# Optimization experiments

Hardware: AMD Instinct MI355X
Metric: run time of the kernel (lower is better)

## Reference

```python
import jax, jax.numpy as jnp
import numpy as np

B = 2
ROW, COL = 63, 84          # resolution
ROW_, COL_ = 32, 42        # resolution_
N = ROW * COL              # 5292 kv tokens
N_ = ROW_ * COL_           # 1344 q tokens
IN_DIM, OUT_DIM = 256, 512
KEY_DIM, NUM_HEADS, ATTN_RATIO, STRIDE = 16, 8, 2, 2
D = ATTN_RATIO * KEY_DIM   # 32 (value dim per head)
DH = D * NUM_HEADS         # 256
NH_KD = KEY_DIM * NUM_HEADS  # 128
H_KV = DH + NH_KD          # 384
SCALE = KEY_DIM ** -0.5
EPS = 1e-5


def _build_bias_idxs():
    # replicates the itertools.product double loop, vectorized; ids ordered by
    # first occurrence in row-major scan (same as dict insertion order).
    r_ = np.arange(ROW_); c_ = np.arange(COL_)
    r = np.arange(ROW); c = np.arange(COL)
    off_r = np.abs(r_[:, None] * STRIDE - r[None, :])      # (32, 63)
    off_c = np.abs(c_[:, None] * STRIDE - c[None, :])      # (42, 84)
    keys = (off_r[:, None, :, None] * 1000 + off_c[None, :, None, :]).reshape(-1)
    _, first_idx, inv = np.unique(keys, return_index=True, return_inverse=True)
    order = np.argsort(first_idx)
    rank = np.empty_like(order); rank[order] = np.arange(len(order))
    idxs = rank[inv].reshape(N_, N).astype(np.int32)
    return idxs, len(order)


def setup_inputs() -> dict:
    key = jax.random.key(0)
    ks = jax.random.split(key, 12)
    idxs_np, n_off = _build_bias_idxs()
    inp = {
        "x": jax.random.normal(ks[0], (B, N, IN_DIM), jnp.float32),
        "kv_w": jax.random.normal(ks[1], (H_KV, IN_DIM), jnp.float32) * (IN_DIM ** -0.5),
        "kv_g": jnp.ones((H_KV,), jnp.float32),
        "kv_b": jnp.zeros((H_KV,), jnp.float32),
        "q_w": jax.random.normal(ks[2], (NH_KD, IN_DIM), jnp.float32) * (IN_DIM ** -0.5),
        "q_g": jnp.ones((NH_KD,), jnp.float32),
        "q_b": jnp.zeros((NH_KD,), jnp.float32),
        "proj_w": jax.random.normal(ks[3], (OUT_DIM, DH), jnp.float32) * (DH ** -0.5),
        "proj_g": jnp.ones((OUT_DIM,), jnp.float32),
        "proj_b": jnp.zeros((OUT_DIM,), jnp.float32),
        "bias_table": jax.random.normal(ks[4], (NUM_HEADS, n_off), jnp.float32) * 0.02,
        "bias_idxs": jnp.asarray(idxs_np),
    }
    return inp


def _linear_bn(x, w, g, b):
    # Linear (no bias) followed by BatchNorm1d in training mode (batch stats
    # over flattened (B*N) dim, biased variance).
    y = jnp.einsum("bnc,oc->bno", x, w)
    flat = y.reshape(-1, y.shape[-1])
    mu = flat.mean(0)
    var = flat.var(0)
    return (y - mu) * (g / jnp.sqrt(var + EPS)) + b


def _hardswish(x):
    return x * jnp.clip(x + 3.0, 0.0, 6.0) / 6.0


def reference(x, kv_w, kv_g, kv_b, q_w, q_g, q_b, proj_w, proj_g, proj_b,
              bias_table, bias_idxs):
    Bx = x.shape[0]
    # kv projection -> split k (KEY_DIM) and v (D) per head
    kv = _linear_bn(x, kv_w, kv_g, kv_b).reshape(Bx, N, NUM_HEADS, KEY_DIM + D)
    k = kv[..., :KEY_DIM].transpose(0, 2, 1, 3)   # (B, H, N, key_dim)
    v = kv[..., KEY_DIM:].transpose(0, 2, 1, 3)   # (B, H, N, d)
    # q: spatial subsample then projection
    xs = x.reshape(Bx, ROW, COL, IN_DIM)[:, ::STRIDE, ::STRIDE].reshape(Bx, N_, IN_DIM)
    q = _linear_bn(xs, q_w, q_g, q_b).reshape(Bx, N_, NUM_HEADS, KEY_DIM).transpose(0, 2, 1, 3)
    # gathered relative position bias: (H, N_, N)
    ab = bias_table[:, bias_idxs]
    attn = jnp.einsum("bhqd,bhkd->bhqk", q, k) * SCALE + ab[None]
    attn = jax.nn.softmax(attn, axis=-1)
    out = jnp.einsum("bhqk,bhkd->bhqd", attn, v)       # (B, H, N_, d)
    out = out.transpose(0, 2, 1, 3).reshape(Bx, N_, DH)
    out = _linear_bn(_hardswish(out), proj_w, proj_g, proj_b)
    return out
```

## Files before the change

### kernel.cpp

```cpp
#include <hip/hip_runtime.h>
#include <hip/hip_bf16.h>
#include <math.h>

#define N_K 5292
#define N_Q 1344
#define NH_KD 128
#define NROWS 21504
#define LOG2E 1.4426950408889634f
#define MSTAT 16.0f

typedef float f32x4 __attribute__((ext_vector_type(4)));
typedef short short8 __attribute__((ext_vector_type(8)));

__device__ __forceinline__ float fexp2(float x) {
#if __has_builtin(__builtin_amdgcn_exp2f)
    return __builtin_amdgcn_exp2f(x);
#else
    return exp2f(x);
#endif
}

__device__ __forceinline__ unsigned pk_bf16(float a, float b) {
    union { __hip_bfloat162 h; unsigned u; } c;
    c.h = __float22bfloat162_rn(make_float2(a, b));
    return c.u;
}
__device__ __forceinline__ unsigned short f2bf(float a) {
    return (unsigned short)pk_bf16(a, 0.f);
}

__global__ __launch_bounds__(256) void prep_kernel(
    const float* __restrict__ x, const float* __restrict__ kv_w,
    const float* __restrict__ q_w, const float* __restrict__ proj_w,
    const float* __restrict__ bias_table, const int* __restrict__ bias_idxs, int n_off,
    float* __restrict__ sums, unsigned short* __restrict__ Xp,
    unsigned short* __restrict__ Wp, float* __restrict__ bt_r)
{
    int bid = blockIdx.x;
    const int t = threadIdx.x;
    if (bid < 8) {
        int i = bid * 256 + t;
        if (i < 2048) sums[i] = 0.f;
        return;
    }
    bid -= 8;
    if (bid < 2646) {
        int i = bid * 256 + t;
        float4 v = ((const float4*)x)[i];
        ((uint2*)Xp)[i] = make_uint2(pk_bf16(v.x, v.y), pk_bf16(v.z, v.w));
        return;
    }
    bid -= 2646;
    if (bid < 256) {
        int i = bid * 256 + t;
        int j = i;
        const float* s;
        if (j < 384 * 64) s = kv_w;
        else if ((j -= 384 * 64) < 128 * 64) s = q_w;
        else { j -= 128 * 64; s = proj_w; }
        float4 v = ((const float4*)s)[j];
        ((uint2*)Wp)[i] = make_uint2(pk_bf16(v.x, v.y), pk_bf16(v.z, v.w));
        return;
    }
    bid -= 256;
    {
        int i = bid * 256 + t;
        if (i < 8 * N_K) {
            int h = i / N_K, j = i - h * N_K;
            bt_r[i] = fmaf(bias_table[h * n_off + bias_idxs[j]], LOG2E, -MSTAT);
        }
    }
}

__device__ __forceinline__ void gemm_body(
    const unsigned short* __restrict__ Ap, const unsigned short* __restrict__ Wp,
    long asrc, int nrow,
    unsigned short (*As)[40], unsigned short (*Bs)[40], f32x4 acc[4])
{
    const int t = threadIdx.x;
    const int w = t >> 6, lane = t & 63, g = lane >> 4, ln = lane & 15;
    const int srow = t >> 2;
    const int sc8 = (t & 3) * 8;

    for (int k0 = 0; k0 < 256; k0 += 32) {
        uint4 a = make_uint4(0, 0, 0, 0);
        if (asrc >= 0) a = *(const uint4*)(Ap + asrc * 256 + k0 + sc8);
        uint4 b = *(const uint4*)(Wp + (size_t)nrow * 256 + k0 + sc8);

        __syncthreads();
        *(uint4*)&As[srow][sc8] = a;
        *(uint4*)&Bs[srow][sc8] = b;
        __syncthreads();

        short8 ah = *(const short8*)&As[w * 16 + ln][g * 8];
        #pragma unroll
        for (int nt = 0; nt < 4; ++nt) {
            short8 bh = *(const short8*)&Bs[nt * 16 + ln][g * 8];
            acc[nt] = __builtin_amdgcn_mfma_f32_16x16x32_bf16(ah, bh, acc[nt], 0, 0, 0);
        }
    }
}

__device__ __forceinline__ void gemm_stats(f32x4 acc[4], float* __restrict__ sums,
                                           int n0, int Ncols, float* scratch)
{
    const int t = threadIdx.x;
    const int w = t >> 6, lane = t & 63, g = lane >> 4, ln = lane & 15;
    float s4[4], q4[4];
    #pragma unroll
    for (int nt = 0; nt < 4; ++nt) {
        float s = acc[nt][0] + acc[nt][1] + acc[nt][2] + acc[nt][3];
        float q = fmaf(acc[nt][0], acc[nt][0], fmaf(acc[nt][1], acc[nt][1],
                  fmaf(acc[nt][2], acc[nt][2], acc[nt][3] * acc[nt][3])));
        s += __shfl_xor(s, 16); s += __shfl_xor(s, 32);
        q += __shfl_xor(q, 16); q += __shfl_xor(q, 32);
        s4[nt] = s; q4[nt] = q;
    }
    __syncthreads();
    float* st_s = scratch;
    float* st_q = scratch + 256;
    if (g == 0) {
        #pragma unroll
        for (int nt = 0; nt < 4; ++nt) {
            st_s[(w * 4 + nt) * 16 + ln] = s4[nt];
            st_q[(w * 4 + nt) * 16 + ln] = q4[nt];
        }
    }
    __syncthreads();
    if (t < 64) {
        int nt = t >> 4, c = t & 15;
        float a = 0.f, b2 = 0.f;
        #pragma unroll
        for (int ww = 0; ww < 4; ++ww) {
            a  += st_s[(ww * 4 + nt) * 16 + c];
            b2 += st_q[(ww * 4 + nt) * 16 + c];
        }
        atomicAdd(&sums[n0 + nt * 16 + c], a);
        atomicAdd(&sums[Ncols + n0 + nt * 16 + c], b2);
    }
}

__global__ __launch_bounds__(256) void gemm_qkv(
    const unsigned short* __restrict__ Xp, const unsigned short* __restrict__ Wp,
    unsigned short* __restrict__ Kp, unsigned short* __restrict__ Vp,
    float* __restrict__ q_y, float* __restrict__ sums_kv, float* __restrict__ sums_q)
{
    __shared__ unsigned short As[64][40], Bs[64][40];
    const int t = threadIdx.x;
    const int w = t >> 6, lane = t & 63, g = lane >> 4, ln = lane & 15;
    const int srow = t >> 2;
    int id = blockIdx.x;

    f32x4 acc[4];
    #pragma unroll
    for (int nt = 0; nt < 4; ++nt) acc[nt] = (f32x4){0.f, 0.f, 0.f, 0.f};

    if (id < 1008) {
        const int xcd = id & 7, id8 = id >> 3;
        const int my = xcd + (id8 / 6) * 8, ny = id8 % 6;
        if (my >= 166) return;
        const int m0 = my * 64, n0 = ny * 64;
        int mrow = m0 + srow;
        long asrc = (mrow < 10584) ? mrow : -1;
        gemm_body(Xp, Wp, asrc, n0 + srow, As, Bs, acc);

        #pragma unroll
        for (int nt = 0; nt < 4; ++nt) {
            int c = n0 + nt * 16 + ln;
            int hh = c / 48, cc = c - 48 * hh;
            #pragma unroll
            for (int reg = 0; reg < 4; ++reg) {
                int mr = m0 + w * 16 + g * 4 + reg;
                if (mr < 10584) {
                    int bb = mr >= N_K;
                    int key = mr - bb * N_K;
                    unsigned short v16 = f2bf(acc[nt][reg]);
                    size_t slot = (size_t)(bb * 8 + hh) * N_K + key;
                    if (cc < 16) Kp[slot * 16 + cc] = v16;
                    else         Vp[slot * 32 + cc - 16] = v16;
                }
            }
        }
        gemm_stats(acc, sums_kv, n0, 384, (float*)&As[0][0]);
    } else {
        id -= 1008;
        const int xcd = id & 7, id8 = id >> 3;
        const int my = xcd + (id8 / 2) * 8, ny = id8 % 2;
        if (my >= 42) return;
        const int m0 = my * 64, n0 = ny * 64;
        int mrow = m0 + srow;
        long asrc = -1;
        {
            int bb = mrow / N_Q;
            int i = mrow - bb * N_Q;
            asrc = (long)(bb * N_K + (i / 42) * 168 + (i % 42) * 2);
        }
        gemm_body(Xp, Wp + 384 * 256, asrc, n0 + srow, As, Bs, acc);

        #pragma unroll
        for (int nt = 0; nt < 4; ++nt)
            #pragma unroll
            for (int reg = 0; reg < 4; ++reg) {
                int mr = m0 + w * 16 + g * 4 + reg;
                q_y[(size_t)mr * 128 + n0 + nt * 16 + ln] = acc[nt][reg];
            }
        gemm_stats(acc, sums_q, n0, 128, (float*)&As[0][0]);
    }
}

__global__ __launch_bounds__(256) void gemm_proj(
    const unsigned short* __restrict__ Ap, const unsigned short* __restrict__ Wp,
    float* __restrict__ Y, float* __restrict__ sums)
{
    __shared__ unsigned short As[64][40], Bs[64][40];
    const int t = threadIdx.x;
    const int w = t >> 6, lane = t & 63, g = lane >> 4, ln = lane & 15;
    const int id = blockIdx.x;
    const int xcd = id & 7, id8 = id >> 3;
    const int my = xcd + (id8 / 8) * 8, ny = id8 % 8;
    if (my >= 42) return;
    const int m0 = my * 64, n0 = ny * 64;

    f32x4 acc[4];
    #pragma unroll
    for (int nt = 0; nt < 4; ++nt) acc[nt] = (f32x4){0.f, 0.f, 0.f, 0.f};
    gemm_body(Ap, Wp, m0 + (t >> 2), n0 + (t >> 2), As, Bs, acc);

    #pragma unroll
    for (int nt = 0; nt < 4; ++nt)
        #pragma unroll
        for (int reg = 0; reg < 4; ++reg) {
            int mr = m0 + w * 16 + g * 4 + reg;
            Y[(size_t)mr * 512 + n0 + nt * 16 + ln] = acc[nt][reg];
        }
    gemm_stats(acc, sums, n0, 512, (float*)&As[0][0]);
}

__global__ __launch_bounds__(256, 5) void attn_mfma(
    const unsigned short* __restrict__ Kp, const unsigned short* __restrict__ Vp,
    const float* __restrict__ q_y, const float* __restrict__ sums_q,
    const float* __restrict__ q_g, const float* __restrict__ q_b,
    const float* __restrict__ sums_kv, const float* __restrict__ kv_g,
    const float* __restrict__ bt_r,
    float* __restrict__ pl, float* __restrict__ pacc)
{
    const int id = blockIdx.x;
    const int h = id & 7;
    const int z = (id >> 3) & 7;
    const int qt = id >> 6;
    const int b = z >> 2, ks = z & 3;
    const int t = threadIdx.x;
    const int w = t >> 6, lane = t & 63, g = lane >> 4, ln = lane & 15;

    __shared__ float bt_s[21 * 84];
    __shared__ unsigned short K_s[2][64][24];
    __shared__ unsigned short Vt_s[2][32][72];
    __shared__ unsigned short P_s[4][16][72];

    const int q0 = qt * 64;
    const int kstart = ks * 1344;
    const int kend = (kstart + 1344 < N_K) ? kstart + 1344 : N_K;
    const int ntiles = (kend - kstart + 63) >> 6;
    const bool tail = (ks == 3);

    const int kr0 = ks * 16;
    const int kr1 = (kend - 1) / 84;
    const int rq2min = (q0 / 42) * 2;
    const int rq2max = ((q0 + 63) / 42) * 2;
    int dr_lo = 0;
    if (rq2min > kr1) dr_lo = rq2min - kr1;
    else if (kr0 > rq2max) dr_lo = kr0 - rq2max;
    int a1 = rq2max - kr0, a2 = kr1 - rq2min;
    int dr_hi = a1 > a2 ? a1 : a2;
    {
        int nb = (dr_hi - dr_lo + 1) * 84;
        const float* src = bt_r + h * N_K + dr_lo * 84;
        for (int j = t; j < nb; j += 256) bt_s[j] = src[j];
    }

    short8 qfrag = (short8)0;
    if (lane < 32) {
        const float invq = 1.f / 2688.f, invk = 1.f / 10584.f;
        const float post = 0.25f * LOG2E;
        const int c0 = h * 16 + g * 8;
        const int ck = h * 48 + g * 8;
        const float* qp = q_y + (size_t)(b * N_Q + q0 + w * 16 + ln) * NH_KD + c0;
        float vv[8];
        #pragma unroll
        for (int j = 0; j < 8; ++j) {
            float mu  = sums_q[c0 + j] * invq;
            float var = fmaf(-mu, mu, sums_q[128 + c0 + j] * invq);
            float s   = q_g[c0 + j] * rsqrtf(var + 1e-5f) * post;
            float vq  = fmaf(qp[j], s, fmaf(-mu, s, q_b[c0 + j] * post));
            float muk = sums_kv[ck + j] * invk;
            float vrk = fmaf(-muk, muk, sums_kv[384 + ck + j] * invk);
            float sk  = kv_g[ck + j] * rsqrtf(vrk + 1e-5f);
            vv[j] = vq * sk;
        }
        union { short8 s; unsigned u[4]; } qf;
        qf.u[0] = pk_bf16(vv[0], vv[1]); qf.u[1] = pk_bf16(vv[2], vv[3]);
        qf.u[2] = pk_bf16(vv[4], vv[5]); qf.u[3] = pk_bf16(vv[6], vv[7]);
        qfrag = qf.s;
    }

    int rq2[4], cq2[4];
    #pragma unroll
    for (int reg = 0; reg < 4; ++reg) {
        int qg = q0 + w * 16 + g * 4 + reg;
        rq2[reg] = (qg / 42) * 2;
        cq2[reg] = (qg % 42) * 2;
    }
    int kr[4], kc[4];
    #pragma unroll
    for (int st = 0; st < 4; ++st) {
        int kg = kstart + st * 16 + ln;
        kr[st] = kg / 84;
        kc[st] = kg - kr[st] * 84;
    }

    const unsigned* kp_base = (const unsigned*)Kp + (size_t)(b * 8 + h) * N_K * 8;
    const unsigned* vp_base = (const unsigned*)Vp + (size_t)(b * 8 + h) * N_K * 16;
    const int skey = t >> 2, schunk = t & 3;
    const int vslot = ((skey & 15) << 2) | (skey >> 4);
    const int v0 = schunk * 8;

    uint2 kreg; uint4 vreg;
    {
        int kg = kstart + skey; if (kg > N_K - 1) kg = N_K - 1;
        kreg = *(const uint2*)(kp_base + (size_t)kg * 8 + schunk * 2);
        vreg = *(const uint4*)(vp_base + (size_t)kg * 16 + schunk * 4);
    }
    *(uint2*)&K_s[0][skey][schunk * 4] = kreg;
    Vt_s[0][v0 + 0][vslot] = (unsigned short)vreg.x;
    Vt_s[0][v0 + 1][vslot] = (unsigned short)(vreg.x >> 16);
    Vt_s[0][v0 + 2][vslot] = (unsigned short)vreg.y;
    Vt_s[0][v0 + 3][vslot] = (unsigned short)(vreg.y >> 16);
    Vt_s[0][v0 + 4][vslot] = (unsigned short)vreg.z;
    Vt_s[0][v0 + 5][vslot] = (unsigned short)(vreg.z >> 16);
    Vt_s[0][v0 + 6][vslot] = (unsigned short)vreg.w;
    Vt_s[0][v0 + 7][vslot] = (unsigned short)(vreg.w >> 16);
    __syncthreads();

    float l[4] = {0.f, 0.f, 0.f, 0.f};
    f32x4 acc0 = {0.f, 0.f, 0.f, 0.f}, acc1 = {0.f, 0.f, 0.f, 0.f};
    const f32x4 zero4 = {0.f, 0.f, 0.f, 0.f};
    int p = 0;

    for (int it = 0; it < ntiles; ++it) {
        const int k0 = kstart + it * 64;
        const bool notlast = (it + 1 < ntiles);
        if (notlast) {
            int kg = k0 + 64 + skey; if (kg > N_K - 1) kg = N_K - 1;
            kreg = *(const uint2*)(kp_base + (size_t)kg * 8 + schunk * 2);
            vreg = *(const uint4*)(vp_base + (size_t)kg * 16 + schunk * 4);
        }

        f32x4 sf[4];
        #pragma unroll
        for (int st = 0; st < 4; ++st) {
            short8 bf = (short8)0;
            if (lane < 32) bf = *(const short8*)&K_s[p][st * 16 + ln][g * 8];
            sf[st] = __builtin_amdgcn_mfma_f32_16x16x32_bf16(qfrag, bf, zero4, 0, 0, 0);
        }

        float pv[4][4];
        #pragma unroll
        for (int st = 0; st < 4; ++st) {
            #pragma unroll
            for (int reg = 0; reg < 4; ++reg) {
                int dr = rq2[reg] - kr[st]; dr = dr < 0 ? -dr : dr;
                int dc = cq2[reg] - kc[st]; dc = dc < 0 ? -dc : dc;
                pv[st][reg] = fexp2(sf[st][reg] + bt_s[(dr - dr_lo) * 84 + dc]);
            }
        }
        if (tail && it == ntiles - 1) {
            #pragma unroll
            for (int st = 0; st < 4; ++st) {
                bool bad = (k0 + st * 16 + ln) >= N_K;
                #pragma unroll
                for (int reg = 0; reg < 4; ++reg)
                    pv[st][reg] = bad ? 0.f : pv[st][reg];
            }
        }

        #pragma unroll
        for (int reg = 0; reg < 4; ++reg) {
            l[reg] += (pv[0][reg] + pv[1][reg]) + (pv[2][reg] + pv[3][reg]);
            uint2 pw = make_uint2(pk_bf16(pv[0][reg], pv[1][reg]),
                                  pk_bf16(pv[2][reg], pv[3][reg]));
            *(uint2*)&P_s[w][g * 4 + reg][4 * ln] = pw;
        }

        #pragma unroll
        for (int kt = 0; kt < 2; ++kt) {
            short8 af = *(const short8*)&P_s[w][ln][g * 8 + kt * 32];
            short8 b0 = *(const short8*)&Vt_s[p][ln][g * 8 + kt * 32];
            short8 b1 = *(const short8*)&Vt_s[p][ln + 16][g * 8 + kt * 32];
            acc0 = __builtin_amdgcn_mfma_f32_16x16x32_bf16(af, b0, acc0, 0, 0, 0);
            acc1 = __builtin_amdgcn_mfma_f32_16x16x32_bf16(af, b1, acc1, 0, 0, 0);
        }

        if (notlast) {
            int q2 = p ^ 1;
            *(uint2*)&K_s[q2][skey][schunk * 4] = kreg;
            Vt_s[q2][v0 + 0][vslot] = (unsigned short)vreg.x;
            Vt_s[q2][v0 + 1][vslot] = (unsigned short)(vreg.x >> 16);
            Vt_s[q2][v0 + 2][vslot] = (unsigned short)vreg.y;
            Vt_s[q2][v0 + 3][vslot] = (unsigned short)(vreg.y >> 16);
            Vt_s[q2][v0 + 4][vslot] = (unsigned short)vreg.z;
            Vt_s[q2][v0 + 5][vslot] = (unsigned short)(vreg.z >> 16);
            Vt_s[q2][v0 + 6][vslot] = (unsigned short)vreg.w;
            Vt_s[q2][v0 + 7][vslot] = (unsigned short)(vreg.w >> 16);
            __syncthreads();
            p = q2;
        }

        #pragma unroll
        for (int st = 0; st < 4; ++st) {
            kc[st] += 64;
            if (kc[st] >= 84) { kc[st] -= 84; kr[st] += 1; }
        }
    }

    #pragma unroll
    for (int reg = 0; reg < 4; ++reg) {
        float s = l[reg];
        s += __shfl_xor(s, 1, 16);
        s += __shfl_xor(s, 2, 16);
        s += __shfl_xor(s, 4, 16);
        s += __shfl_xor(s, 8, 16);
        l[reg] = s;
    }

    const int rbase = (b * 8 + h) * N_Q + q0 + w * 16;
    #pragma unroll
    for (int reg = 0; reg < 4; ++reg) {
        int prow = ks * NROWS + rbase + g * 4 + reg;
        pacc[(size_t)prow * 32 + ln]      = acc0[reg];
        pacc[(size_t)prow * 32 + 16 + ln] = acc1[reg];
        if (ln == 0) pl[prow] = l[reg];
    }
}

__global__ __launch_bounds__(256) void combine_kernel(const float* __restrict__ pl,
                                                      const float* __restrict__ pacc,
                                                      const float* __restrict__ sums_kv,
                                                      const float* __restrict__ kv_g,
                                                      const float* __restrict__ kv_b,
                                                      unsigned short* __restrict__ attn_o)
{
    int i = blockIdx.x * 256 + threadIdx.x;
    int r = i >> 5, e = i & 31;
    float L = (pl[r] + pl[NROWS + r]) + (pl[2 * NROWS + r] + pl[3 * NROWS + r]);
    float v = (pacc[(size_t)r * 32 + e] + pacc[(size_t)(NROWS + r) * 32 + e])
            + (pacc[(size_t)(2 * NROWS + r) * 32 + e] + pacc[(size_t)(3 * NROWS + r) * 32 + e]);
    int q = r % N_Q;
    int bh = r / N_Q;
    int hh = bh & 7, b = bh >> 3;
    const int ch = hh * 48 + 16 + e;
    const float invk = 1.f / 10584.f;
    float mu  = sums_kv[ch] * invk;
    float var = fmaf(-mu, mu, sums_kv[384 + ch] * invk);
    float s   = kv_g[ch] * rsqrtf(var + 1e-5f);
    float tt  = fmaf(-mu, s, kv_b[ch]);
    v = fmaf(s, v / L, tt);
    float hs = v * fminf(fmaxf(v + 3.f, 0.f), 6.f) * (1.f / 6.f);
    attn_o[(size_t)(b * N_Q + q) * 256 + hh * 32 + e] = f2bf(hs);
}

__global__ __launch_bounds__(256) void norm_apply(
    const float* __restrict__ Y, const float* __restrict__ sums,
    const float* __restrict__ g, const float* __restrict__ bb,
    float* __restrict__ out, int rows, int cols, float inv_rows)
{
    __shared__ float sc_s[64], sh_s[64];
    const int t = threadIdx.x;
    const int c0 = blockIdx.x * 64;
    if (t < 64) {
        int c = c0 + t;
        float mu  = sums[c] * inv_rows;
        float var = fmaf(-mu, mu, sums[cols + c] * inv_rows);
        float s   = g[c] * rsqrtf(var + 1e-5f);
        sc_s[t] = s;
        sh_s[t] = fmaf(-mu, s, bb[c]);
    }
    __syncthreads();
    const int c4 = (t & 15) * 4;
    float4 scv = *(const float4*)&sc_s[c4];
    float4 shv = *(const float4*)&sh_s[c4];
    for (int r = blockIdx.y * 16 + (t >> 4); r < rows; r += gridDim.y * 16) {
        size_t off = (size_t)r * cols + c0 + c4;
        float4 v = *(const float4*)(Y + off);
        v.x = fmaf(v.x, scv.x, shv.x);
        v.y = fmaf(v.y, scv.y, shv.y);
        v.z = fmaf(v.z, scv.z, shv.z);
        v.w = fmaf(v.w, scv.w, shv.w);
        *(float4*)(out + off) = v;
    }
}

extern "C" void kernel_launch(void* const* d_in, const int* in_sizes, int n_in,
                              void* d_out, int out_size, void* d_ws, size_t ws_size,
                              hipStream_t stream) {
    (void)n_in; (void)out_size; (void)ws_size;
    const float* x      = (const float*)d_in[0];
    const float* kv_w   = (const float*)d_in[1];
    const float* kv_g   = (const float*)d_in[2];
    const float* kv_b   = (const float*)d_in[3];
    const float* q_w    = (const float*)d_in[4];
    const float* q_g    = (const float*)d_in[5];
    const float* q_b    = (const float*)d_in[6];
    const float* proj_w = (const float*)d_in[7];
    const float* proj_g = (const float*)d_in[8];
    const float* proj_b = (const float*)d_in[9];
    const float* bias_table = (const float*)d_in[10];
    const int*   bias_idxs  = (const int*)d_in[11];
    const int    n_off = in_sizes[10] / 8;
    float* out = (float*)d_out;

    float* ws = (float*)d_ws;
    float* q_y  = ws;
    float* pacc = q_y + 2688 * 128;
    float* proj_y = pacc;
    float* pl = pacc + 4 * NROWS * 32;
    unsigned short* Xp = (unsigned short*)(pl + 4 * NROWS);
    unsigned short* Wp = Xp + 10584 * 256;
    unsigned short* attn_o = Wp + 1024 * 256;
    unsigned short* Kp = attn_o + 2688 * 256;
    unsigned short* Vp = Kp + 2 * 8 * N_K * 16;
    float* sums_kv = (float*)(Vp + 2 * 8 * N_K * 32);
    float* sums_q  = sums_kv + 768;
    float* sums_p  = sums_q + 256;
    float* bt_r    = sums_p + 1024;

    prep_kernel<<<3076, 256, 0, stream>>>(x, kv_w, q_w, proj_w, bias_table, bias_idxs,
                                          n_off, sums_kv, Xp, Wp, bt_r);
    gemm_qkv<<<1104, 256, 0, stream>>>(Xp, Wp, Kp, Vp, q_y, sums_kv, sums_q);
    attn_mfma<<<1344, 256, 0, stream>>>(Kp, Vp, q_y, sums_q, q_g, q_b,
                                        sums_kv, kv_g, bt_r, pl, pacc);
    combine_kernel<<<2688, 256, 0, stream>>>(pl, pacc, sums_kv, kv_g, kv_b, attn_o);
    gemm_proj<<<8 * 6 * 8, 256, 0, stream>>>(attn_o, Wp + 512 * 256, proj_y, sums_p);
    norm_apply<<<dim3(8, 84), 256, 0, stream>>>(proj_y, sums_p, proj_g, proj_b, out,
                                                2688, 512, 1.f / 2688.f);
}
```

Baseline: 210.6 us.

## Fuse bf16 casts into GEMMs, pre-transpose V, fold combine into attention

Removes the separate fp32-to-bf16 conversion of x and the weights from the prep kernel. The GEMMs now load fp32 and pack to bf16 in registers, which cuts one full read and write of x. The qkv GEMM epilogue writes V already transposed and permuted into a padded key layout, so the attention kernel can stage V with vector stores instead of scalar scatter into shared memory. The separate combine kernel is replaced by a last-block-done counter in the attention kernel, which then reduces the split-K partials and applies BN plus hardswish. This trades a launch and extra traffic for atomics, threadfences, and a scattered transposed V write.

New measurement: 341.6 us. 62.2% more time.

```diff
diff --git a/kernel.cpp b/kernel.cpp
--- a/kernel.cpp
+++ b/kernel.cpp
@@ -3,6 +3,7 @@
 #include <math.h>
 
 #define N_K 5292
+#define N_KP 5376
 #define N_Q 1344
 #define NH_KD 128
 #define NROWS 21504
@@ -30,39 +31,17 @@
 }
 
 __global__ __launch_bounds__(256) void prep_kernel(
-    const float* __restrict__ x, const float* __restrict__ kv_w,
-    const float* __restrict__ q_w, const float* __restrict__ proj_w,
     const float* __restrict__ bias_table, const int* __restrict__ bias_idxs, int n_off,
-    float* __restrict__ sums, unsigned short* __restrict__ Xp,
-    unsigned short* __restrict__ Wp, float* __restrict__ bt_r)
+    float* __restrict__ zbase, float* __restrict__ bt_r)
 {
     int bid = blockIdx.x;
     const int t = threadIdx.x;
-    if (bid < 8) {
+    if (bid < 10) {
         int i = bid * 256 + t;
-        if (i < 2048) sums[i] = 0.f;
+        if (i < 2560) zbase[i] = 0.f;
         return;
     }
-    bid -= 8;
-    if (bid < 2646) {
-        int i = bid * 256 + t;
-        float4 v = ((const float4*)x)[i];
-        ((uint2*)Xp)[i] = make_uint2(pk_bf16(v.x, v.y), pk_bf16(v.z, v.w));
-        return;
-    }
-    bid -= 2646;
-    if (bid < 256) {
-        int i = bid * 256 + t;
-        int j = i;
-        const float* s;
-        if (j < 384 * 64) s = kv_w;
-        else if ((j -= 384 * 64) < 128 * 64) s = q_w;
-        else { j -= 128 * 64; s = proj_w; }
-        float4 v = ((const float4*)s)[j];
-        ((uint2*)Wp)[i] = make_uint2(pk_bf16(v.x, v.y), pk_bf16(v.z, v.w));
-        return;
-    }
-    bid -= 256;
+    bid -= 10;
     {
         int i = bid * 256 + t;
         if (i < 8 * N_K) {
@@ -72,8 +51,8 @@
     }
 }
 
-__device__ __forceinline__ void gemm_body(
-    const unsigned short* __restrict__ Ap, const unsigned short* __restrict__ Wp,
+__device__ __forceinline__ void gemm_body_f32(
+    const float* __restrict__ A, const float* __restrict__ W,
     long asrc, int nrow,
     unsigned short (*As)[40], unsigned short (*Bs)[40], f32x4 acc[4])
 {
@@ -84,8 +63,47 @@
 
     for (int k0 = 0; k0 < 256; k0 += 32) {
         uint4 a = make_uint4(0, 0, 0, 0);
-        if (asrc >= 0) a = *(const uint4*)(Ap + asrc * 256 + k0 + sc8);
-        uint4 b = *(const uint4*)(Wp + (size_t)nrow * 256 + k0 + sc8);
+        if (asrc >= 0) {
+            float4 a0 = *(const float4*)(A + asrc * 256 + k0 + sc8);
+            float4 a1 = *(const float4*)(A + asrc * 256 + k0 + sc8 + 4);
+            a = make_uint4(pk_bf16(a0.x, a0.y), pk_bf16(a0.z, a0.w),
+                           pk_bf16(a1.x, a1.y), pk_bf16(a1.z, a1.w));
+        }
+        float4 b0 = *(const float4*)(W + (size_t)nrow * 256 + k0 + sc8);
+        float4 b1 = *(const float4*)(W + (size_t)nrow * 256 + k0 + sc8 + 4);
+        uint4 b = make_uint4(pk_bf16(b0.x, b0.y), pk_bf16(b0.z, b0.w),
+                             pk_bf16(b1.x, b1.y), pk_bf16(b1.z, b1.w));
+
+        __syncthreads();
+        *(uint4*)&As[srow][sc8] = a;
+        *(uint4*)&Bs[srow][sc8] = b;
+        __syncthreads();
+
+        short8 ah = *(const short8*)&As[w * 16 + ln][g * 8];
+        #pragma unroll
+        for (int nt = 0; nt < 4; ++nt) {
+            short8 bh = *(const short8*)&Bs[nt * 16 + ln][g * 8];
+            acc[nt] = __builtin_amdgcn_mfma_f32_16x16x32_bf16(ah, bh, acc[nt], 0, 0, 0);
+        }
+    }
+}
+
+__device__ __forceinline__ void gemm_body_bf16(
+    const unsigned short* __restrict__ A, const float* __restrict__ W,
+    long asrc, int nrow,
+    unsigned short (*As)[40], unsigned short (*Bs)[40], f32x4 acc[4])
+{
+    const int t = threadIdx.x;
+    const int w = t >> 6, lane = t & 63, g = lane >> 4, ln = lane & 15;
+    const int srow = t >> 2;
+    const int sc8 = (t & 3) * 8;
+
+    for (int k0 = 0; k0 < 256; k0 += 32) {
+        uint4 a = *(const uint4*)(A + asrc * 256 + k0 + sc8);
+        float4 b0 = *(const float4*)(W + (size_t)nrow * 256 + k0 + sc8);
+        float4 b1 = *(const float4*)(W + (size_t)nrow * 256 + k0 + sc8 + 4);
+        uint4 b = make_uint4(pk_bf16(b0.x, b0.y), pk_bf16(b0.z, b0.w),
+                             pk_bf16(b1.x, b1.y), pk_bf16(b1.z, b1.w));
 
         __syncthreads();
         *(uint4*)&As[srow][sc8] = a;
@@ -141,8 +159,8 @@
 }
 
 __global__ __launch_bounds__(256) void gemm_qkv(
-    const unsigned short* __restrict__ Xp, const unsigned short* __restrict__ Wp,
-    unsigned short* __restrict__ Kp, unsigned short* __restrict__ Vp,
+    const float* __restrict__ X, const float* __restrict__ kv_w, const float* __restrict__ q_w,
+    unsigned short* __restrict__ Kp, unsigned short* __restrict__ Vpt,
     float* __restrict__ q_y, float* __restrict__ sums_kv, float* __restrict__ sums_q)
 {
     __shared__ unsigned short As[64][40], Bs[64][40];
@@ -162,7 +180,7 @@
         const int m0 = my * 64, n0 = ny * 64;
         int mrow = m0 + srow;
         long asrc = (mrow < 10584) ? mrow : -1;
-        gemm_body(Xp, Wp, asrc, n0 + srow, As, Bs, acc);
+        gemm_body_f32(X, kv_w, asrc, n0 + srow, As, Bs, acc);
 
         #pragma unroll
         for (int nt = 0; nt < 4; ++nt) {
@@ -175,9 +193,13 @@
                     int bb = mr >= N_K;
                     int key = mr - bb * N_K;
                     unsigned short v16 = f2bf(acc[nt][reg]);
-                    size_t slot = (size_t)(bb * 8 + hh) * N_K + key;
-                    if (cc < 16) Kp[slot * 16 + cc] = v16;
-                    else         Vp[slot * 32 + cc - 16] = v16;
+                    if (cc < 16) {
+                        Kp[((size_t)(bb * 8 + hh) * N_K + key) * 16 + cc] = v16;
+                    } else {
+                        int kap = key & 63;
+                        int keyp = (key & ~63) | (((kap & 15) << 2) | (kap >> 4));
+                        Vpt[((size_t)(bb * 8 + hh) * 32 + cc - 16) * N_KP + keyp] = v16;
+                    }
                 }
             }
         }
@@ -189,13 +211,10 @@
         if (my >= 42) return;
         const int m0 = my * 64, n0 = ny * 64;
         int mrow = m0 + srow;
-        long asrc = -1;
-        {
-            int bb = mrow / N_Q;
-            int i = mrow - bb * N_Q;
-            asrc = (long)(bb * N_K + (i / 42) * 168 + (i % 42) * 2);
-        }
-        gemm_body(Xp, Wp + 384 * 256, asrc, n0 + srow, As, Bs, acc);
+        int bb = mrow / N_Q;
+        int i = mrow - bb * N_Q;
+        long asrc = (long)(bb * N_K + (i / 42) * 168 + (i % 42) * 2);
+        gemm_body_f32(X, q_w, asrc, n0 + srow, As, Bs, acc);
 
         #pragma unroll
         for (int nt = 0; nt < 4; ++nt)
@@ -209,7 +228,7 @@
 }
 
 __global__ __launch_bounds__(256) void gemm_proj(
-    const unsigned short* __restrict__ Ap, const unsigned short* __restrict__ Wp,
+    const unsigned short* __restrict__ Ap, const float* __restrict__ Wp,
     float* __restrict__ Y, float* __restrict__ sums)
 {
     __shared__ unsigned short As[64][40], Bs[64][40];
@@ -224,7 +243,7 @@
     f32x4 acc[4];
     #pragma unroll
     for (int nt = 0; nt < 4; ++nt) acc[nt] = (f32x4){0.f, 0.f, 0.f, 0.f};
-    gemm_body(Ap, Wp, m0 + (t >> 2), n0 + (t >> 2), As, Bs, acc);
+    gemm_body_bf16(Ap, Wp, m0 + (t >> 2), n0 + (t >> 2), As, Bs, acc);
 
     #pragma unroll
     for (int nt = 0; nt < 4; ++nt)
@@ -237,12 +256,13 @@
 }
 
 __global__ __launch_bounds__(256, 5) void attn_mfma(
-    const unsigned short* __restrict__ Kp, const unsigned short* __restrict__ Vp,
+    const unsigned short* __restrict__ Kp, const unsigned short* __restrict__ Vpt,
     const float* __restrict__ q_y, const float* __restrict__ sums_q,
     const float* __restrict__ q_g, const float* __restrict__ q_b,
     const float* __restrict__ sums_kv, const float* __restrict__ kv_g,
-    const float* __restrict__ bt_r,
-    float* __restrict__ pl, float* __restrict__ pacc)
+    const float* __restrict__ kv_b, const float* __restrict__ bt_r,
+    float* __restrict__ pl, float* __restrict__ pacc,
+    int* __restrict__ counters, unsigned short* __restrict__ attn_o)
 {
     const int id = blockIdx.x;
     const int h = id & 7;
@@ -253,9 +273,10 @@
     const int w = t >> 6, lane = t & 63, g = lane >> 4, ln = lane & 15;
 
     __shared__ float bt_s[21 * 84];
-    __shared__ unsigned short K_s[2][64][24];
-    __shared__ unsigned short Vt_s[2][32][72];
+    __shared__ unsigned short K_s[2][64][26];
+    __shared__ unsigned short Vt_s[2][32][66];
     __shared__ unsigned short P_s[4][16][72];
+    __shared__ int s_win;
 
     const int q0 = qt * 64;
     const int kstart = ks * 1344;
@@ -319,26 +340,18 @@
     }
 
     const unsigned* kp_base = (const unsigned*)Kp + (size_t)(b * 8 + h) * N_K * 8;
-    const unsigned* vp_base = (const unsigned*)Vp + (size_t)(b * 8 + h) * N_K * 16;
+    const unsigned short* vp_base = Vpt + (size_t)(b * 8 + h) * 32 * N_KP;
     const int skey = t >> 2, schunk = t & 3;
-    const int vslot = ((skey & 15) << 2) | (skey >> 4);
-    const int v0 = schunk * 8;
+    const int vrow = t >> 3, vc8 = (t & 7) * 8;
 
     uint2 kreg; uint4 vreg;
     {
         int kg = kstart + skey; if (kg > N_K - 1) kg = N_K - 1;
         kreg = *(const uint2*)(kp_base + (size_t)kg * 8 + schunk * 2);
-        vreg = *(const uint4*)(vp_base + (size_t)kg * 16 + schunk * 4);
+        vreg = *(const uint4*)(vp_base + (size_t)vrow * N_KP + kstart + vc8);
     }
     *(uint2*)&K_s[0][skey][schunk * 4] = kreg;
-    Vt_s[0][v0 + 0][vslot] = (unsigned short)vreg.x;
-    Vt_s[0][v0 + 1][vslot] = (unsigned short)(vreg.x >> 16);
-    Vt_s[0][v0 + 2][vslot] = (unsigned short)vreg.y;
-    Vt_s[0][v0 + 3][vslot] = (unsigned short)(vreg.y >> 16);
-    Vt_s[0][v0 + 4][vslot] = (unsigned short)vreg.z;
-    Vt_s[0][v0 + 5][vslot] = (unsigned short)(vreg.z >> 16);
-    Vt_s[0][v0 + 6][vslot] = (unsigned short)vreg.w;
-    Vt_s[0][v0 + 7][vslot] = (unsigned short)(vreg.w >> 16);
+    *(uint4*)&Vt_s[0][vrow][vc8] = vreg;
     __syncthreads();
 
     float l[4] = {0.f, 0.f, 0.f, 0.f};
@@ -352,7 +365,7 @@
         if (notlast) {
             int kg = k0 + 64 + skey; if (kg > N_K - 1) kg = N_K - 1;
             kreg = *(const uint2*)(kp_base + (size_t)kg * 8 + schunk * 2);
-            vreg = *(const uint4*)(vp_base + (size_t)kg * 16 + schunk * 4);
+            vreg = *(const uint4*)(vp_base + (size_t)vrow * N_KP + k0 + 64 + vc8);
         }
 
         f32x4 sf[4];
@@ -403,14 +416,7 @@
         if (notlast) {
             int q2 = p ^ 1;
             *(uint2*)&K_s[q2][skey][schunk * 4] = kreg;
-            Vt_s[q2][v0 + 0][vslot] = (unsigned short)vreg.x;
-            Vt_s[q2][v0 + 1][vslot] = (unsigned short)(vreg.x >> 16);
-            Vt_s[q2][v0 + 2][vslot] = (unsigned short)vreg.y;
-            Vt_s[q2][v0 + 3][vslot] = (unsigned short)(vreg.y >> 16);
-            Vt_s[q2][v0 + 4][vslot] = (unsigned short)vreg.z;
-            Vt_s[q2][v0 + 5][vslot] = (unsigned short)(vreg.z >> 16);
-            Vt_s[q2][v0 + 6][vslot] = (unsigned short)vreg.w;
-            Vt_s[q2][v0 + 7][vslot] = (unsigned short)(vreg.w >> 16);
+            *(uint4*)&Vt_s[q2][vrow][vc8] = vreg;
             __syncthreads();
             p = q2;
         }
@@ -440,32 +446,43 @@
         pacc[(size_t)prow * 32 + 16 + ln] = acc1[reg];
         if (ln == 0) pl[prow] = l[reg];
     }
-}
-
-__global__ __launch_bounds__(256) void combine_kernel(const float* __restrict__ pl,
-                                                      const float* __restrict__ pacc,
-                                                      const float* __restrict__ sums_kv,
-                                                      const float* __restrict__ kv_g,
-                                                      const float* __restrict__ kv_b,
-                                                      unsigned short* __restrict__ attn_o)
-{
-    int i = blockIdx.x * 256 + threadIdx.x;
-    int r = i >> 5, e = i & 31;
-    float L = (pl[r] + pl[NROWS + r]) + (pl[2 * NROWS + r] + pl[3 * NROWS + r]);
-    float v = (pacc[(size_t)r * 32 + e] + pacc[(size_t)(NROWS + r) * 32 + e])
-            + (pacc[(size_t)(2 * NROWS + r) * 32 + e] + pacc[(size_t)(3 * NROWS + r) * 32 + e]);
-    int q = r % N_Q;
-    int bh = r / N_Q;
-    int hh = bh & 7, b = bh >> 3;
-    const int ch = hh * 48 + 16 + e;
+
+    __threadfence();
+    if (t == 0) {
+        int old = atomicAdd(&counters[(qt * 2 + b) * 8 + h], 1);
+        s_win = (old == 3);
+    }
+    __syncthreads();
+    if (!s_win) return;
+    __threadfence();
+
+    const int cq = t >> 2, e8 = (t & 3) * 8;
+    const int row = (b * 8 + h) * N_Q + q0 + cq;
+    float L = (pl[row] + pl[NROWS + row]) + (pl[2 * NROWS + row] + pl[3 * NROWS + row]);
+    float invL = 1.f / L;
     const float invk = 1.f / 10584.f;
-    float mu  = sums_kv[ch] * invk;
-    float var = fmaf(-mu, mu, sums_kv[384 + ch] * invk);
-    float s   = kv_g[ch] * rsqrtf(var + 1e-5f);
-    float tt  = fmaf(-mu, s, kv_b[ch]);
-    v = fmaf(s, v / L, tt);
-    float hs = v * fminf(fmaxf(v + 3.f, 0.f), 6.f) * (1.f / 6.f);
-    attn_o[(size_t)(b * N_Q + q) * 256 + hh * 32 + e] = f2bf(hs);
+    unsigned outw[4];
+    #pragma unroll
+    for (int jp = 0; jp < 4; ++jp) {
+        float vj[2];
+        #pragma unroll
+        for (int u = 0; u < 2; ++u) {
+            int e = e8 + jp * 2 + u;
+            size_t o = (size_t)row * 32 + e;
+            float v = (pacc[o] + pacc[(size_t)NROWS * 32 + o])
+                    + (pacc[(size_t)2 * NROWS * 32 + o] + pacc[(size_t)3 * NROWS * 32 + o]);
+            int ch = h * 48 + 16 + e;
+            float mu  = sums_kv[ch] * invk;
+            float var = fmaf(-mu, mu, sums_kv[384 + ch] * invk);
+            float s   = kv_g[ch] * rsqrtf(var + 1e-5f);
+            float tt  = fmaf(-mu, s, kv_b[ch]);
+            v = fmaf(s, v * invL, tt);
+            vj[u] = v * fminf(fmaxf(v + 3.f, 0.f), 6.f) * (1.f / 6.f);
+        }
+        outw[jp] = pk_bf16(vj[0], vj[1]);
+    }
+    *(uint4*)(attn_o + (size_t)(b * N_Q + q0 + cq) * 256 + h * 32 + e8) =
+        make_uint4(outw[0], outw[1], outw[2], outw[3]);
 }
 
 __global__ __launch_bounds__(256) void norm_apply(
@@ -523,23 +540,22 @@
     float* pacc = q_y + 2688 * 128;
     float* proj_y = pacc;
     float* pl = pacc + 4 * NROWS * 32;
-    unsigned short* Xp = (unsigned short*)(pl + 4 * NROWS);
-    unsigned short* Wp = Xp + 10584 * 256;
-    unsigned short* attn_o = Wp + 1024 * 256;
-    unsigned short* Kp = attn_o + 2688 * 256;
-    unsigned short* Vp = Kp + 2 * 8 * N_K * 16;
-    float* sums_kv = (float*)(Vp + 2 * 8 * N_K * 32);
+    unsigned short* attn_o = (unsigned short*)(pl + 4 * NROWS);
+    unsigned short* Kp  = attn_o + 2688 * 256;
+    unsigned short* Vpt = Kp + 2 * 8 * N_K * 16;
+    float* zbase   = (float*)(Vpt + 2 * 8 * 32 * N_KP);
+    float* sums_kv = zbase;
     float* sums_q  = sums_kv + 768;
     float* sums_p  = sums_q + 256;
-    float* bt_r    = sums_p + 1024;
-
-    prep_kernel<<<3076, 256, 0, stream>>>(x, kv_w, q_w, proj_w, bias_table, bias_idxs,
-                                          n_off, sums_kv, Xp, Wp, bt_r);
-    gemm_qkv<<<1104, 256, 0, stream>>>(Xp, Wp, Kp, Vp, q_y, sums_kv, sums_q);
-    attn_mfma<<<1344, 256, 0, stream>>>(Kp, Vp, q_y, sums_q, q_g, q_b,
-                                        sums_kv, kv_g, bt_r, pl, pacc);
-    combine_kernel<<<2688, 256, 0, stream>>>(pl, pacc, sums_kv, kv_g, kv_b, attn_o);
-    gemm_proj<<<8 * 6 * 8, 256, 0, stream>>>(attn_o, Wp + 512 * 256, proj_y, sums_p);
+    int*   counters = (int*)(sums_p + 1024);
+    float* bt_r    = (float*)(counters + 512);
+
+    prep_kernel<<<176, 256, 0, stream>>>(bias_table, bias_idxs, n_off, zbase, bt_r);
+    gemm_qkv<<<1104, 256, 0, stream>>>(x, kv_w, q_w, Kp, Vpt, q_y, sums_kv, sums_q);
+    attn_mfma<<<1344, 256, 0, stream>>>(Kp, Vpt, q_y, sums_q, q_g, q_b,
+                                        sums_kv, kv_g, kv_b, bt_r, pl, pacc,
+                                        counters, attn_o);
+    gemm_proj<<<384, 256, 0, stream>>>(attn_o, proj_w, proj_y, sums_p);
     norm_apply<<<dim3(8, 84), 256, 0, stream>>>(proj_y, sums_p, proj_g, proj_b, out,
                                                 2688, 512, 1.f / 2688.f);
 }
```
